# Kernel tuning notes

Measured on AMD Instinct MI355X. Metric: run time of the kernel, lower is better.

The kernel has to match this reference:

```python
import jax, jax.numpy as jnp
import numpy as np

NUM_SRC = 100000
NUM_DST = 100000
NUM_EDGES = 800000
WIDTH = 128
LEAKY_SLOPE = 0.01  # torch LeakyReLU default


def setup_inputs() -> dict:
    key = jax.random.key(0)
    k1, k2, k3, k4 = jax.random.split(key, 4)
    x_src = jax.random.normal(k1, (NUM_SRC, WIDTH), dtype=jnp.float32)
    x_dst = jax.random.normal(k2, (NUM_DST, WIDTH), dtype=jnp.float32)
    e = jax.random.randint(k3, (2, NUM_EDGES), 0, NUM_DST, dtype=jnp.int64)
    W = jax.random.normal(k4, (2 * WIDTH, WIDTH), dtype=jnp.float32) * 0.02
    b = jnp.zeros((WIDTH,), dtype=jnp.float32)
    return {"x_src": x_src, "x_dst": x_dst, "e": e, "W": W, "b": b}


def reference(x_src, x_dst, e, W, b):
    src_idx, dst_idx = e[0], e[1]
    # gather + per-edge diff: [E, W]
    diffs = x_dst[dst_idx] - x_src[src_idx]
    # segment max over destination nodes; empty segments -> 0 (matches torch.zeros_like init)
    seg_max = jax.ops.segment_max(diffs, dst_idx, num_segments=NUM_DST)
    counts = jax.ops.segment_sum(jnp.ones((diffs.shape[0],), dtype=x_dst.dtype),
                                 dst_idx, num_segments=NUM_DST)
    maxes = jnp.where(counts[:, None] > 0, seg_max, jnp.zeros_like(seg_max))
    # MLP: Linear(2W -> W) + LeakyReLU, then residual
    h = jnp.concatenate([x_dst, maxes], axis=1) @ W + b
    h = jax.nn.leaky_relu(h, negative_slope=LEAKY_SLOPE)
    return x_dst + h
```

## Files before the change

kernel.cpp:

```cpp
#include <hip/hip_runtime.h>

#define WIDTH 128
#define SLOPE 0.01f
#define SBS 512
#define FBM 16
#define ECAP 512

typedef __attribute__((ext_vector_type(8))) short short8;
typedef __attribute__((ext_vector_type(4))) float f32x4;

__device__ __forceinline__ unsigned short f2bf(float f) {
    unsigned b = __float_as_uint(f);
    b += 0x7FFFu + ((b >> 16) & 1u);
    return (unsigned short)(b >> 16);
}
__device__ __forceinline__ float4 upk(uint2 u) {
    float4 r;
    r.x = __uint_as_float(u.x << 16);
    r.y = __uint_as_float(u.x & 0xFFFF0000u);
    r.z = __uint_as_float(u.y << 16);
    r.w = __uint_as_float(u.y & 0xFFFF0000u);
    return r;
}
__device__ __forceinline__ unsigned short map16(unsigned short x) {
    return (x & 0x8000u) ? (unsigned short)(~x) : (unsigned short)(x | 0x8000u);
}
__device__ __forceinline__ unsigned short unmap16(unsigned u) {
    return (unsigned short)((u & 0x8000u) ? (u ^ 0x8000u) : (~u & 0xFFFFu));
}
__device__ __forceinline__ unsigned pkmin(unsigned a, unsigned b) {
    unsigned r;
    asm("v_pk_min_u16 %0, %1, %2" : "=v"(r) : "v"(a), "v"(b));
    return r;
}
__device__ __forceinline__ uint4 pk4(uint4 a, uint4 b) {
    uint4 r;
    r.x = pkmin(a.x, b.x);
    r.y = pkmin(a.y, b.y);
    r.z = pkmin(a.z, b.z);
    r.w = pkmin(a.w, b.w);
    return r;
}
__device__ __forceinline__ int swz(int lr, int bc) {
    return lr * 512 + (bc ^ ((lr & 7) << 4));
}

__global__ void prep_kernel(const float* __restrict__ x_src,
                            const float* __restrict__ W,
                            const int* __restrict__ e,
                            unsigned short* __restrict__ xsb,
                            unsigned short* __restrict__ Wt,
                            unsigned* __restrict__ counts,
                            int* __restrict__ rank,
                            int NS, int E, int nconv, int nhist) {
    int b = blockIdx.x;
    if (b < nconv) {
        int i = b * 256 + threadIdx.x;
        if (i < NS * 32) {
            float4 v = reinterpret_cast<const float4*>(x_src)[i];
            ushort4 o;
            o.x = map16(f2bf(v.x)); o.y = map16(f2bf(v.y));
            o.z = map16(f2bf(v.z)); o.w = map16(f2bf(v.w));
            *reinterpret_cast<ushort4*>(xsb + (size_t)i * 4) = o;
        }
    } else if (b < nconv + nhist) {
        int i = (b - nconv) * 256 + threadIdx.x;
        if (i < E) {
            int dst = e[E + i];
            rank[i] = (int)atomicAdd(&counts[dst], 1u);
        }
    } else {
        int t = (b - nconv - nhist) * 256 + threadIdx.x;
        if (t < 128 * 64) {
            int n = t & 127, kc = t >> 7;
            ushort4 o;
            unsigned short* op = &o.x;
            #pragma unroll
            for (int j = 0; j < 4; ++j) {
                int k = kc * 4 + j;
                float v;
                if (k < 128) v = W[(size_t)k * 128 + n] + W[(size_t)(k + 128) * 128 + n];
                else         v = -W[(size_t)k * 128 + n];
                op[j] = f2bf(v);
            }
            *reinterpret_cast<ushort4*>(Wt + (size_t)n * 256 + kc * 4) = o;
        }
    }
}

__global__ void block_sum_kernel(const unsigned* __restrict__ counts,
                                 unsigned* __restrict__ bsums, int M) {
    int i = blockIdx.x * SBS + threadIdx.x;
    unsigned v = (i < M) ? counts[i] : 0u;
    for (int d = 32; d > 0; d >>= 1) v += __shfl_down(v, d);
    __shared__ unsigned ws[SBS / 64];
    int lane = threadIdx.x & 63, w = threadIdx.x >> 6;
    if (lane == 0) ws[w] = v;
    __syncthreads();
    if (threadIdx.x == 0) {
        unsigned s = 0;
        for (int k = 0; k < SBS / 64; ++k) s += ws[k];
        bsums[blockIdx.x] = s;
    }
}

__global__ void bsum_scan_kernel(const unsigned* __restrict__ bsums,
                                 unsigned* __restrict__ bbase, int NB,
                                 int* __restrict__ offsets, int M) {
    __shared__ unsigned s[256];
    int t = threadIdx.x;
    unsigned v = (t < NB) ? bsums[t] : 0u;
    s[t] = v;
    __syncthreads();
    for (int off = 1; off < 256; off <<= 1) {
        unsigned n = (t >= off) ? s[t - off] : 0u;
        __syncthreads();
        s[t] += n;
        __syncthreads();
    }
    if (t < NB) bbase[t] = s[t] - v;
    if (t == 255) offsets[M] = (int)s[255];
}

__global__ void scan_final_kernel(const unsigned* __restrict__ counts,
                                  const unsigned* __restrict__ bbase,
                                  int* __restrict__ offsets, int M) {
    int b = blockIdx.x, t = threadIdx.x;
    int i = b * SBS + t;
    unsigned c = (i < M) ? counts[i] : 0u;
    unsigned v = c;
    int lane = t & 63, w = t >> 6;
    for (int d = 1; d < 64; d <<= 1) {
        unsigned n = __shfl_up(v, d);
        if (lane >= d) v += n;
    }
    __shared__ unsigned ws[SBS / 64];
    if (lane == 63) ws[w] = v;
    __syncthreads();
    unsigned wbase = 0;
    for (int k = 0; k < w; ++k) wbase += ws[k];
    if (i < M) offsets[i] = (int)(bbase[b] + wbase + v - c);
}

__global__ void scatter_kernel(const int* __restrict__ e,
                               const int* __restrict__ offsets,
                               const int* __restrict__ rank,
                               int* __restrict__ csr, int E) {
    int i = blockIdx.x * blockDim.x + threadIdx.x;
    if (i < E) {
        int dst = e[E + i];
        csr[offsets[dst] + rank[i]] = e[i];
    }
}

template<int XSB>
__global__ __launch_bounds__(256, 4) void fused_kernel(
        const float* __restrict__ x_src,
        const unsigned short* __restrict__ xsb,
        const float* __restrict__ x_dst,
        const int* __restrict__ offsets,
        const int* __restrict__ csr,
        const unsigned short* __restrict__ Wt,
        const float* __restrict__ bias,
        float* __restrict__ out, int M) {
    __shared__ __align__(16) unsigned short At[FBM * 256];
    __shared__ __align__(16) int eidx[ECAP];
    __shared__ int offs[FBM + 1];
    char* Ab = reinterpret_cast<char*>(At);
    int tid = threadIdx.x;
    int lane = tid & 63;
    int wv = tid >> 6;
    int blockRow = blockIdx.x * FBM;

    int ebeg = offsets[blockRow];
    int eend = offsets[blockRow + FBM];
    int ecount = eend - ebeg;
    if (tid <= FBM) offs[tid] = offsets[blockRow + tid];
    #pragma unroll
    for (int i = 0; i < FBM * 32 / 256; ++i) {
        int u = tid + 256 * i;
        int lr = u >> 5, c4 = u & 31;
        float4 v = reinterpret_cast<const float4*>(x_dst)[(size_t)(blockRow + lr) * 32 + c4];
        ushort4 o;
        o.x = f2bf(v.x); o.y = f2bf(v.y); o.z = f2bf(v.z); o.w = f2bf(v.w);
        *reinterpret_cast<ushort4*>(Ab + swz(lr, c4 * 8)) = o;
    }
    bool fit = (ecount <= ECAP);
    for (int i = tid; i < min(ecount, ECAP); i += 256) eidx[i] = csr[ebeg + i];
    __syncthreads();

    int l15 = lane & 15;
    int rg = lane >> 4;
    int lr = wv * 4 + rg;
    int rb = offs[lr] - ebeg;
    int re = offs[lr + 1] - ebeg;
    int deg = re - rb;
    int lim = re - 1;
    int oA = offs[wv * 4], oB = offs[wv * 4 + 1], oC = offs[wv * 4 + 2];
    int oD = offs[wv * 4 + 3], oE = offs[wv * 4 + 4];
    int mb = max(max(oB - oA, oC - oB), max(oD - oC, oE - oD));

    uint4 mnv = make_uint4(~0u, ~0u, ~0u, ~0u);

    if (XSB) {
        if (mb > 0) {
            const uint4* xs = reinterpret_cast<const uint4*>(xsb);
            int ix[16];
            #pragma unroll
            for (int j = 0; j < 16; ++j) {
                int p = max(min(rb + j, lim), 0);
                ix[j] = fit ? eidx[p] : csr[ebeg + p];
            }
            uint4 v[16];
            #pragma unroll
            for (int j = 0; j < 16; ++j) v[j] = xs[(size_t)ix[j] * 16 + l15];
            #pragma unroll
            for (int s = 8; s >= 1; s >>= 1)
                #pragma unroll
                for (int j = 0; j < s; ++j) v[j] = pk4(v[j], v[j + s]);
            mnv = v[0];
            for (int e0 = 16; e0 < mb; e0 += 8) {
                uint4 t[8];
                #pragma unroll
                for (int j = 0; j < 8; ++j) {
                    int p = max(min(rb + e0 + j, lim), 0);
                    int iv = fit ? eidx[p] : csr[ebeg + p];
                    t[j] = xs[(size_t)iv * 16 + l15];
                }
                #pragma unroll
                for (int s = 4; s >= 1; s >>= 1)
                    #pragma unroll
                    for (int j = 0; j < s; ++j) t[j] = pk4(t[j], t[j + s]);
                mnv = pk4(mnv, t[0]);
            }
        }
    } else {
        float mn[8];
        #pragma unroll
        for (int j = 0; j < 8; ++j) mn[j] = INFINITY;
        const float4* xf = reinterpret_cast<const float4*>(x_src);
        for (int e0 = 0; e0 < mb; e0 += 2) {
            int p0 = max(min(rb + e0 + 0, lim), 0);
            int p1 = max(min(rb + e0 + 1, lim), 0);
            int i0 = fit ? eidx[p0] : csr[ebeg + p0];
            int i1 = fit ? eidx[p1] : csr[ebeg + p1];
            float4 a0 = xf[(size_t)i0 * 32 + l15 * 2];
            float4 b0 = xf[(size_t)i0 * 32 + l15 * 2 + 1];
            float4 a1 = xf[(size_t)i1 * 32 + l15 * 2];
            float4 b1 = xf[(size_t)i1 * 32 + l15 * 2 + 1];
            mn[0] = fminf(mn[0], fminf(a0.x, a1.x));
            mn[1] = fminf(mn[1], fminf(a0.y, a1.y));
            mn[2] = fminf(mn[2], fminf(a0.z, a1.z));
            mn[3] = fminf(mn[3], fminf(a0.w, a1.w));
            mn[4] = fminf(mn[4], fminf(b0.x, b1.x));
            mn[5] = fminf(mn[5], fminf(b0.y, b1.y));
            mn[6] = fminf(mn[6], fminf(b0.z, b1.z));
            mn[7] = fminf(mn[7], fminf(b0.w, b1.w));
        }
        mnv.x = (unsigned)map16(f2bf(mn[0])) | ((unsigned)map16(f2bf(mn[1])) << 16);
        mnv.y = (unsigned)map16(f2bf(mn[2])) | ((unsigned)map16(f2bf(mn[3])) << 16);
        mnv.z = (unsigned)map16(f2bf(mn[4])) | ((unsigned)map16(f2bf(mn[5])) << 16);
        mnv.w = (unsigned)map16(f2bf(mn[6])) | ((unsigned)map16(f2bf(mn[7])) << 16);
    }

    {
        ushort4 oa, ob;
        if (deg > 0) {
            oa.x = unmap16(mnv.x & 0xFFFFu); oa.y = unmap16(mnv.x >> 16);
            oa.z = unmap16(mnv.y & 0xFFFFu); oa.w = unmap16(mnv.y >> 16);
            ob.x = unmap16(mnv.z & 0xFFFFu); ob.y = unmap16(mnv.z >> 16);
            ob.z = unmap16(mnv.w & 0xFFFFu); ob.w = unmap16(mnv.w >> 16);
        } else {
            oa = *reinterpret_cast<const ushort4*>(Ab + swz(lr, l15 * 16));
            ob = *reinterpret_cast<const ushort4*>(Ab + swz(lr, l15 * 16 + 8));
        }
        *reinterpret_cast<ushort4*>(Ab + swz(lr, 256 + l15 * 16)) = oa;
        *reinterpret_cast<ushort4*>(Ab + swz(lr, 256 + l15 * 16 + 8)) = ob;
    }
    __syncthreads();

    int q = lane >> 4;
    int ncol0 = wv * 32;
    f32x4 acc0 = (f32x4){0.f, 0.f, 0.f, 0.f};
    f32x4 acc1 = (f32x4){0.f, 0.f, 0.f, 0.f};
    size_t b0off = (size_t)(ncol0 + l15) * 256;
    size_t b1off = (size_t)(ncol0 + 16 + l15) * 256;

    #pragma unroll
    for (int s = 0; s < 8; ++s) {
        int koff = s * 32 + q * 8;
        short8 b0 = *reinterpret_cast<const short8*>(Wt + b0off + koff);
        short8 b1 = *reinterpret_cast<const short8*>(Wt + b1off + koff);
        short8 a = *reinterpret_cast<const short8*>(Ab + swz(l15, koff * 2));
        acc0 = __builtin_amdgcn_mfma_f32_16x16x32_bf16(b0, a, acc0, 0, 0, 0);
        acc1 = __builtin_amdgcn_mfma_f32_16x16x32_bf16(b1, a, acc1, 0, 0, 0);
    }

    float4 bi0 = *reinterpret_cast<const float4*>(bias + ncol0 + q * 4);
    float4 bi1 = *reinterpret_cast<const float4*>(bias + ncol0 + 16 + q * 4);
    int row = blockRow + l15;
    #pragma unroll
    for (int u = 0; u < 2; ++u) {
        int col = ncol0 + u * 16 + q * 4;
        f32x4 av = u ? acc1 : acc0;
        float4 bv = u ? bi1 : bi0;
        uint2 xu = *reinterpret_cast<const uint2*>(Ab + swz(l15, col * 2));
        float4 xb = upk(xu);
        float4 o;
        float h;
        h = av[0] + bv.x; o.x = xb.x + (h > 0.f ? h : SLOPE * h);
        h = av[1] + bv.y; o.y = xb.y + (h > 0.f ? h : SLOPE * h);
        h = av[2] + bv.z; o.z = xb.z + (h > 0.f ? h : SLOPE * h);
        h = av[3] + bv.w; o.w = xb.w + (h > 0.f ? h : SLOPE * h);
        *reinterpret_cast<float4*>(out + (size_t)row * 128 + col) = o;
    }
}

extern "C" void kernel_launch(void* const* d_in, const int* in_sizes, int n_in,
                              void* d_out, int out_size, void* d_ws, size_t ws_size,
                              hipStream_t stream) {
    const float* x_src = (const float*)d_in[0];
    const float* x_dst = (const float*)d_in[1];
    const int*   e     = (const int*)d_in[2];
    const float* W     = (const float*)d_in[3];
    const float* bias  = (const float*)d_in[4];
    float* out = (float*)d_out;

    int NS = in_sizes[0] / WIDTH;
    int E  = in_sizes[2] / 2;
    int M  = in_sizes[1] / WIDTH;
    int NB = (M + SBS - 1) / SBS;

    unsigned short* xsb = (unsigned short*)d_ws;
    unsigned short* Wt  = xsb + (size_t)NS * WIDTH;
    unsigned* counts  = (unsigned*)(Wt + 128 * 256);
    int*      offsets = (int*)(counts + M);
    int*      rank    = offsets + (M + 1);
    int*      csr     = rank + E;
    unsigned* bsums   = (unsigned*)(csr + E);
    unsigned* bbase   = bsums + NB;
    size_t need = (char*)(bbase + NB) - (char*)d_ws;
    int use_xsb = (ws_size >= need) ? 1 : 0;
    if (!use_xsb) {
        Wt = (unsigned short*)d_ws;
        counts  = (unsigned*)(Wt + 128 * 256);
        offsets = (int*)(counts + M);
        rank    = offsets + (M + 1);
        csr     = rank + E;
        bsums   = (unsigned*)(csr + E);
        bbase   = bsums + NB;
    }

    hipMemsetAsync(counts, 0, (size_t)M * sizeof(unsigned), stream);

    int nconv = use_xsb ? (NS * 32 + 255) / 256 : 0;
    int nhist = (E + 255) / 256;
    int nwt   = (128 * 64 + 255) / 256;
    prep_kernel<<<nconv + nhist + nwt, 256, 0, stream>>>(x_src, W, e, xsb, Wt,
                                                         counts, rank, NS, E,
                                                         nconv, nhist);
    block_sum_kernel<<<NB, SBS, 0, stream>>>(counts, bsums, M);
    bsum_scan_kernel<<<1, 256, 0, stream>>>(bsums, bbase, NB, offsets, M);
    scan_final_kernel<<<NB, SBS, 0, stream>>>(counts, bbase, offsets, M);
    scatter_kernel<<<(E + 255) / 256, 256, 0, stream>>>(e, offsets, rank, csr, E);

    int fblocks = (M + FBM - 1) / FBM;
    if (use_xsb)
        fused_kernel<1><<<fblocks, 256, 0, stream>>>(x_src, xsb, x_dst, offsets,
                                                     csr, Wt, bias, out, M);
    else
        fused_kernel<0><<<fblocks, 256, 0, stream>>>(x_src, xsb, x_dst, offsets,
                                                     csr, Wt, bias, out, M);
}
```

Baseline: 146.9 us.

## Gather each destination row with a full wave using wave-uniform edge indices

The segment-min gather now assigns one whole wave to each destination row, two rows at a time, with each lane loading one 32-bit word (two bf16 values). Previously 16 lanes shared a row and each loaded 16 bytes. Edge indices are read straight from the CSR array and made wave-uniform with readfirstlane, which removes the shared-memory index staging, its capacity check and one block barrier. The aim is fully coalesced row loads and less LDS and synchronisation overhead. In exchange each wave issues about four times as many, narrower gather load instructions, and padding rows to 16 edges still repeats loads of the same data.

Measured after the change: 154.7 us. 5.3% more time.

```diff
diff --git a/kernel.cpp b/kernel.cpp
--- a/kernel.cpp
+++ b/kernel.cpp
@@ -4,7 +4,6 @@
 #define SLOPE 0.01f
 #define SBS 512
 #define FBM 16
-#define ECAP 512
 
 typedef __attribute__((ext_vector_type(8))) short short8;
 typedef __attribute__((ext_vector_type(4))) float f32x4;
@@ -31,14 +30,6 @@
 __device__ __forceinline__ unsigned pkmin(unsigned a, unsigned b) {
     unsigned r;
     asm("v_pk_min_u16 %0, %1, %2" : "=v"(r) : "v"(a), "v"(b));
-    return r;
-}
-__device__ __forceinline__ uint4 pk4(uint4 a, uint4 b) {
-    uint4 r;
-    r.x = pkmin(a.x, b.x);
-    r.y = pkmin(a.y, b.y);
-    r.z = pkmin(a.z, b.z);
-    r.w = pkmin(a.w, b.w);
     return r;
 }
 __device__ __forceinline__ int swz(int lr, int bc) {
@@ -162,20 +153,13 @@
         const int* __restrict__ csr,
         const unsigned short* __restrict__ Wt,
         const float* __restrict__ bias,
-        float* __restrict__ out, int M) {
+        float* __restrict__ out, int M, int E) {
     __shared__ __align__(16) unsigned short At[FBM * 256];
-    __shared__ __align__(16) int eidx[ECAP];
-    __shared__ int offs[FBM + 1];
     char* Ab = reinterpret_cast<char*>(At);
     int tid = threadIdx.x;
     int lane = tid & 63;
-    int wv = tid >> 6;
     int blockRow = blockIdx.x * FBM;
 
-    int ebeg = offsets[blockRow];
-    int eend = offsets[blockRow + FBM];
-    int ecount = eend - ebeg;
-    if (tid <= FBM) offs[tid] = offsets[blockRow + tid];
     #pragma unroll
     for (int i = 0; i < FBM * 32 / 256; ++i) {
         int u = tid + 256 * i;
@@ -185,102 +169,88 @@
         o.x = f2bf(v.x); o.y = f2bf(v.y); o.z = f2bf(v.z); o.w = f2bf(v.w);
         *reinterpret_cast<ushort4*>(Ab + swz(lr, c4 * 8)) = o;
     }
-    bool fit = (ecount <= ECAP);
-    for (int i = tid; i < min(ecount, ECAP); i += 256) eidx[i] = csr[ebeg + i];
-    __syncthreads();
-
-    int l15 = lane & 15;
-    int rg = lane >> 4;
-    int lr = wv * 4 + rg;
-    int rb = offs[lr] - ebeg;
-    int re = offs[lr + 1] - ebeg;
-    int deg = re - rb;
-    int lim = re - 1;
-    int oA = offs[wv * 4], oB = offs[wv * 4 + 1], oC = offs[wv * 4 + 2];
-    int oD = offs[wv * 4 + 3], oE = offs[wv * 4 + 4];
-    int mb = max(max(oB - oA, oC - oB), max(oD - oC, oE - oD));
-
-    uint4 mnv = make_uint4(~0u, ~0u, ~0u, ~0u);
-
-    if (XSB) {
-        if (mb > 0) {
-            const uint4* xs = reinterpret_cast<const uint4*>(xsb);
-            int ix[16];
+
+    int wvu = __builtin_amdgcn_readfirstlane(tid >> 6);
+    int rbase = blockRow + wvu * 4;
+    int off[5];
+    #pragma unroll
+    for (int k = 0; k < 5; ++k)
+        off[k] = __builtin_amdgcn_readfirstlane(offsets[rbase + k]);
+    int Elast = E - 1;
+    const unsigned* xs = reinterpret_cast<const unsigned*>(xsb);
+
+    unsigned outw[4];
+    #pragma unroll
+    for (int pr = 0; pr < 2; ++pr) {
+        unsigned va[16], vb[16];
+        int begA = off[pr * 2 + 0], endA = off[pr * 2 + 1];
+        int begB = off[pr * 2 + 1], endB = off[pr * 2 + 2];
+        int degA = endA - begA, degB = endB - begB;
+        int limA = min(max(endA - 1, begA), Elast);
+        int limB = min(max(endB - 1, begB), Elast);
+        if (XSB) {
             #pragma unroll
             for (int j = 0; j < 16; ++j) {
-                int p = max(min(rb + j, lim), 0);
-                ix[j] = fit ? eidx[p] : csr[ebeg + p];
-            }
-            uint4 v[16];
-            #pragma unroll
-            for (int j = 0; j < 16; ++j) v[j] = xs[(size_t)ix[j] * 16 + l15];
+                int pA = min(begA + j, limA);
+                int iA = __builtin_amdgcn_readfirstlane(csr[pA]);
+                va[j] = xs[(size_t)(unsigned)iA * 64u + lane];
+                int pB = min(begB + j, limB);
+                int iB = __builtin_amdgcn_readfirstlane(csr[pB]);
+                vb[j] = xs[(size_t)(unsigned)iB * 64u + lane];
+            }
             #pragma unroll
             for (int s = 8; s >= 1; s >>= 1)
                 #pragma unroll
-                for (int j = 0; j < s; ++j) v[j] = pk4(v[j], v[j + s]);
-            mnv = v[0];
-            for (int e0 = 16; e0 < mb; e0 += 8) {
-                uint4 t[8];
-                #pragma unroll
-                for (int j = 0; j < 8; ++j) {
-                    int p = max(min(rb + e0 + j, lim), 0);
-                    int iv = fit ? eidx[p] : csr[ebeg + p];
-                    t[j] = xs[(size_t)iv * 16 + l15];
+                for (int j = 0; j < s; ++j) {
+                    va[j] = pkmin(va[j], va[j + s]);
+                    vb[j] = pkmin(vb[j], vb[j + s]);
                 }
-                #pragma unroll
-                for (int s = 4; s >= 1; s >>= 1)
-                    #pragma unroll
-                    for (int j = 0; j < s; ++j) t[j] = pk4(t[j], t[j + s]);
-                mnv = pk4(mnv, t[0]);
-            }
+            unsigned mnA = va[0], mnB = vb[0];
+            for (int e0 = 16; e0 < degA; ++e0) {
+                int idx = __builtin_amdgcn_readfirstlane(csr[begA + e0]);
+                mnA = pkmin(mnA, xs[(size_t)(unsigned)idx * 64u + lane]);
+            }
+            for (int e0 = 16; e0 < degB; ++e0) {
+                int idx = __builtin_amdgcn_readfirstlane(csr[begB + e0]);
+                mnB = pkmin(mnB, xs[(size_t)(unsigned)idx * 64u + lane]);
+            }
+            outw[pr * 2 + 0] = (unsigned)unmap16(mnA & 0xFFFFu)
+                             | ((unsigned)unmap16(mnA >> 16) << 16);
+            outw[pr * 2 + 1] = (unsigned)unmap16(mnB & 0xFFFFu)
+                             | ((unsigned)unmap16(mnB >> 16) << 16);
+        } else {
+            const float2* xf = reinterpret_cast<const float2*>(x_src);
+            float2 mA = make_float2(INFINITY, INFINITY);
+            float2 mB = mA;
+            for (int e0 = 0; e0 < degA; ++e0) {
+                int idx = __builtin_amdgcn_readfirstlane(csr[begA + e0]);
+                float2 v = xf[(size_t)idx * 64 + lane];
+                mA.x = fminf(mA.x, v.x); mA.y = fminf(mA.y, v.y);
+            }
+            for (int e0 = 0; e0 < degB; ++e0) {
+                int idx = __builtin_amdgcn_readfirstlane(csr[begB + e0]);
+                float2 v = xf[(size_t)idx * 64 + lane];
+                mB.x = fminf(mB.x, v.x); mB.y = fminf(mB.y, v.y);
+            }
+            outw[pr * 2 + 0] = (unsigned)f2bf(mA.x) | ((unsigned)f2bf(mA.y) << 16);
+            outw[pr * 2 + 1] = (unsigned)f2bf(mB.x) | ((unsigned)f2bf(mB.y) << 16);
         }
-    } else {
-        float mn[8];
-        #pragma unroll
-        for (int j = 0; j < 8; ++j) mn[j] = INFINITY;
-        const float4* xf = reinterpret_cast<const float4*>(x_src);
-        for (int e0 = 0; e0 < mb; e0 += 2) {
-            int p0 = max(min(rb + e0 + 0, lim), 0);
-            int p1 = max(min(rb + e0 + 1, lim), 0);
-            int i0 = fit ? eidx[p0] : csr[ebeg + p0];
-            int i1 = fit ? eidx[p1] : csr[ebeg + p1];
-            float4 a0 = xf[(size_t)i0 * 32 + l15 * 2];
-            float4 b0 = xf[(size_t)i0 * 32 + l15 * 2 + 1];
-            float4 a1 = xf[(size_t)i1 * 32 + l15 * 2];
-            float4 b1 = xf[(size_t)i1 * 32 + l15 * 2 + 1];
-            mn[0] = fminf(mn[0], fminf(a0.x, a1.x));
-            mn[1] = fminf(mn[1], fminf(a0.y, a1.y));
-            mn[2] = fminf(mn[2], fminf(a0.z, a1.z));
-            mn[3] = fminf(mn[3], fminf(a0.w, a1.w));
-            mn[4] = fminf(mn[4], fminf(b0.x, b1.x));
-            mn[5] = fminf(mn[5], fminf(b0.y, b1.y));
-            mn[6] = fminf(mn[6], fminf(b0.z, b1.z));
-            mn[7] = fminf(mn[7], fminf(b0.w, b1.w));
-        }
-        mnv.x = (unsigned)map16(f2bf(mn[0])) | ((unsigned)map16(f2bf(mn[1])) << 16);
-        mnv.y = (unsigned)map16(f2bf(mn[2])) | ((unsigned)map16(f2bf(mn[3])) << 16);
-        mnv.z = (unsigned)map16(f2bf(mn[4])) | ((unsigned)map16(f2bf(mn[5])) << 16);
-        mnv.w = (unsigned)map16(f2bf(mn[6])) | ((unsigned)map16(f2bf(mn[7])) << 16);
-    }
-
-    {
-        ushort4 oa, ob;
-        if (deg > 0) {
-            oa.x = unmap16(mnv.x & 0xFFFFu); oa.y = unmap16(mnv.x >> 16);
-            oa.z = unmap16(mnv.y & 0xFFFFu); oa.w = unmap16(mnv.y >> 16);
-            ob.x = unmap16(mnv.z & 0xFFFFu); ob.y = unmap16(mnv.z >> 16);
-            ob.z = unmap16(mnv.w & 0xFFFFu); ob.w = unmap16(mnv.w >> 16);
-        } else {
-            oa = *reinterpret_cast<const ushort4*>(Ab + swz(lr, l15 * 16));
-            ob = *reinterpret_cast<const ushort4*>(Ab + swz(lr, l15 * 16 + 8));
-        }
-        *reinterpret_cast<ushort4*>(Ab + swz(lr, 256 + l15 * 16)) = oa;
-        *reinterpret_cast<ushort4*>(Ab + swz(lr, 256 + l15 * 16 + 8)) = ob;
+    }
+
+    #pragma unroll
+    for (int r = 0; r < 4; ++r) {
+        int lr = wvu * 4 + r;
+        int deg = off[r + 1] - off[r];
+        unsigned o = outw[r];
+        if (deg == 0)
+            o = *reinterpret_cast<const unsigned*>(Ab + swz(lr, lane * 4));
+        *reinterpret_cast<unsigned*>(Ab + swz(lr, 256 + lane * 4)) = o;
     }
     __syncthreads();
 
+    int l15 = lane & 15;
     int q = lane >> 4;
-    int ncol0 = wv * 32;
+    int ncol0 = wvu * 32;
     f32x4 acc0 = (f32x4){0.f, 0.f, 0.f, 0.f};
     f32x4 acc1 = (f32x4){0.f, 0.f, 0.f, 0.f};
     size_t b0off = (size_t)(ncol0 + l15) * 256;
@@ -367,8 +337,8 @@
     int fblocks = (M + FBM - 1) / FBM;
     if (use_xsb)
         fused_kernel<1><<<fblocks, 256, 0, stream>>>(x_src, xsb, x_dst, offsets,
-                                                     csr, Wt, bias, out, M);
+                                                     csr, Wt, bias, out, M, E);
     else
         fused_kernel<0><<<fblocks, 256, 0, stream>>>(x_src, xsb, x_dst, offsets,
-                                                     csr, Wt, bias, out, M);
-}
+                                                     csr, Wt, bias, out, M, E);
+}
```
